# Kernel tuning notes

Measured on AMD Instinct MI355X. Metric: run time of the kernel, lower is better.

The kernel has to match this reference:

```python
import jax, jax.numpy as jnp
import numpy as np

T, H, B = 1024, 512, 64

def setup_inputs() -> dict:
    key = jax.random.key(0)
    ks = jax.random.split(key, 9)
    s = 1.0 / np.sqrt(H)
    inp = {"in_seq": jax.random.normal(ks[0], (T, H, B), dtype=jnp.float32)}
    for i, name in enumerate(["Wxi", "Wxf", "Wxo", "Wxg", "Whi", "Whf", "Who", "Whg"]):
        inp[name] = jax.random.normal(ks[i + 1], (H, H), dtype=jnp.float32) * s
    return inp


def reference(in_seq, Wxi, Wxf, Wxo, Wxg, Whi, Whf, Who, Whg):
    # in_seq: [T, H, B]; x_t, h_t, c_t: [H, B]
    h0 = jnp.zeros_like(in_seq[0])
    c0 = jnp.zeros_like(in_seq[0])

    def step(carry, x):
        h, c = carry
        i = jax.nn.sigmoid(Wxi @ x + Whi @ h)
        f = jax.nn.sigmoid(Wxf @ x + Whf @ h)
        g = jnp.tanh(Wxg @ x + Whg @ h)
        o = jax.nn.sigmoid(Wxo @ x + Who @ h)
        c = f * c + i * g
        h = o * jnp.tanh(c)
        return (h, c), h

    (h, c), outputs = jax.lax.scan(step, (h0, c0), in_seq)
    return outputs, h, c  # outputs: [T, H, B]
```

## Files before the change

kernel.cpp:

```cpp
#include <hip/hip_runtime.h>
#include <hip/hip_bf16.h>

typedef unsigned short u16;
typedef unsigned int   u32;
typedef unsigned long long u64;

typedef __attribute__((ext_vector_type(8))) short short8;
typedef __attribute__((ext_vector_type(4))) float f32x4;
typedef __attribute__((ext_vector_type(4))) u32   u32x4;

#define TT 1024
#define HH 512
#define BB 64
#define GCOLS 8
#define LDSK 528

#define HTB_PAR 16384
#define HTB_GRP 2048

__device__ __forceinline__ u16 f2bf(float f) {
    union { float f; u32 u; } v; v.f = f;
    u32 u = v.u;
    return (u16)((u + 0x7FFFu + ((u >> 16) & 1u)) >> 16);
}

__device__ __forceinline__ short8 cvt8(const float4 &a, const float4 &b) {
    short8 r;
    r[0] = (short)f2bf(a.x); r[1] = (short)f2bf(a.y);
    r[2] = (short)f2bf(a.z); r[3] = (short)f2bf(a.w);
    r[4] = (short)f2bf(b.x); r[5] = (short)f2bf(b.y);
    r[6] = (short)f2bf(b.z); r[7] = (short)f2bf(b.w);
    return r;
}

__device__ __forceinline__ float fast_rcp(float x) {
    float r; asm("v_rcp_f32 %0, %1" : "=v"(r) : "v"(x)); return r;
}
__device__ __forceinline__ float fast_sigmoid(float x) {
    return fast_rcp(1.f + __expf(-x));
}
__device__ __forceinline__ float fast_tanh(float x) {
    float e = __expf(2.f * x);
    return 1.f - 2.f * fast_rcp(e + 1.f);
}

__device__ __forceinline__ void barrier_lgkm() {
    asm volatile("s_waitcnt lgkmcnt(0)" ::: "memory");
    __builtin_amdgcn_s_barrier();
}

__device__ __forceinline__ void load4_llc(const u64* p, u32x4 &A, u32x4 &B, u32x4 &C, u32x4 &D) {
    asm volatile(
        "global_load_dwordx4 %0, %4, off sc0 sc1\n\t"
        "global_load_dwordx4 %1, %4, off offset:16 sc0 sc1\n\t"
        "global_load_dwordx4 %2, %4, off offset:32 sc0 sc1\n\t"
        "global_load_dwordx4 %3, %4, off offset:48 sc0 sc1\n\t"
        "s_waitcnt vmcnt(0)"
        : "=&v"(A), "=&v"(B), "=&v"(C), "=&v"(D) : "v"(p) : "memory");
}
__device__ __forceinline__ void store_llc(u64* p, u64 v) {
    asm volatile("global_store_dwordx2 %0, %1, off sc0 sc1" :: "v"(p), "v"(v) : "memory");
}

__global__ void lstm_prep(u64* htb) {
    int i = blockIdx.x * 256 + threadIdx.x;
    __hip_atomic_store(&htb[i], 0ull, __ATOMIC_RELAXED, __HIP_MEMORY_SCOPE_AGENT);
}

__global__ __launch_bounds__(256, 1)
void lstm_persist(const float* __restrict__ in_seq,
                  const float* __restrict__ Wxi, const float* __restrict__ Wxf,
                  const float* __restrict__ Wxo, const float* __restrict__ Wxg,
                  const float* __restrict__ Whi, const float* __restrict__ Whf,
                  const float* __restrict__ Who, const float* __restrict__ Whg,
                  float* __restrict__ out, u64* htb)
{
    __shared__ u16 xt[2][16][LDSK];
    __shared__ u16 htl[16][LDSK];

    const int tid  = threadIdx.x;
    const int bid  = blockIdx.x;
    const int g    = bid & 7;
    const int rblk = bid >> 3;
    const int wave = tid >> 6;
    const int lane = tid & 63;
    const int lrow = lane & 15;
    const int lk8  = (lane >> 4) * 8;

    {
        u16* p0 = &xt[0][0][0]; u16* p1 = &htl[0][0];
        for (int i = tid; i < 2 * 16 * LDSK; i += 256) p0[i] = 0;
        for (int i = tid; i < 16 * LDSK; i += 256) p1[i] = 0;
    }

    const int gt   = lrow & 3;
    const int grow = rblk * 16 + wave * 4 + (lrow >> 2);
    const float* WxS = (gt == 0) ? Wxi : (gt == 1) ? Wxf : (gt == 2) ? Wxo : Wxg;
    const float* WhS = (gt == 0) ? Whi : (gt == 1) ? Whf : (gt == 2) ? Who : Whg;

    short8 afrag[32];
    #pragma unroll
    for (int kk = 0; kk < 16; ++kk) {
        const float* s = WxS + grow * HH + kk * 32 + lk8;
        afrag[kk] = cvt8(*(const float4*)s, *(const float4*)(s + 4));
    }
    #pragma unroll
    for (int kk = 0; kk < 16; ++kk) {
        const float* s = WhS + grow * HH + kk * 32 + lk8;
        afrag[16 + kk] = cvt8(*(const float4*)s, *(const float4*)(s + 4));
    }

    const int q    = lane >> 4;
    const int colv = lrow;
    const int hid  = rblk * 16 + wave * 4 + q;
    float cst = 0.f;
    float hv_prev = 0.f;

    const int sc   = tid >> 5;
    const int sk0  = (tid & 31) * 16;
    const int soff = g * HTB_GRP + sc * 256 + (tid & 31) * 8;
    const int doff = g * HTB_GRP + colv * 256 + (hid >> 1);

    float4 a0, a1, b0, b1;
    {
        const float* xb = in_seq + (size_t)(tid * 2) * BB + g * GCOLS;
        a0 = *(const float4*)(xb);      a1 = *(const float4*)(xb + 4);
        b0 = *(const float4*)(xb + BB); b1 = *(const float4*)(xb + BB + 4);
        int k = tid * 2;
        const float *ra = (const float*)&a0, *rb = (const float*)&b0;
        #pragma unroll
        for (int j = 0; j < 4; ++j)
            *(u32*)&xt[0][j][k] = (u32)f2bf(ra[j]) | ((u32)f2bf(rb[j]) << 16);
        const float *ra1 = (const float*)&a1, *rb1 = (const float*)&b1;
        #pragma unroll
        for (int j = 0; j < 4; ++j)
            *(u32*)&xt[0][4 + j][k] = (u32)f2bf(ra1[j]) | ((u32)f2bf(rb1[j]) << 16);
    }
    __syncthreads();

    for (int t = 0; t < TT; ++t) {
        f32x4 aA = {0.f, 0.f, 0.f, 0.f}, aB = {0.f, 0.f, 0.f, 0.f};
        {
            const u16 (*xc)[LDSK] = xt[t & 1];
            #pragma unroll
            for (int kk = 0; kk < 8; ++kk) {
                short8 bfr = *(const short8*)&xc[lrow][kk * 32 + lk8];
                aA = __builtin_amdgcn_mfma_f32_16x16x32_bf16(afrag[kk], bfr, aA, 0, 0, 0);
            }
            #pragma unroll
            for (int kk = 8; kk < 16; ++kk) {
                short8 bfr = *(const short8*)&xc[lrow][kk * 32 + lk8];
                aB = __builtin_amdgcn_mfma_f32_16x16x32_bf16(afrag[kk], bfr, aB, 0, 0, 0);
            }
        }

        if (t > 0) {
            const u64* pC = htb + (t & 1) * HTB_PAR + soff;
            const u32 want = (u32)t;
            u32x4 A, B, C, D;
            bool got = false;
            do {
                load4_llc(pC, A, B, C, D);
                got = (A[1] == want) & (A[3] == want) & (B[1] == want) & (B[3] == want) &
                      (C[1] == want) & (C[3] == want) & (D[1] == want) & (D[3] == want);
            } while (!got);

            if (colv < 8)
                out[(size_t)(t - 1) * (HH * BB) + hid * BB + g * GCOLS + colv] = hv_prev;

            u32x4 lo, hi;
            lo[0] = A[0]; lo[1] = A[2]; lo[2] = B[0]; lo[3] = B[2];
            hi[0] = C[0]; hi[1] = C[2]; hi[2] = D[0]; hi[3] = D[2];
            *(u32x4*)&htl[sc][sk0]     = lo;
            *(u32x4*)&htl[sc][sk0 + 8] = hi;
        }

        if (t + 1 < TT) {
            const float* xb = in_seq + (size_t)(t + 1) * (HH * BB)
                            + (size_t)(tid * 2) * BB + g * GCOLS;
            a0 = *(const float4*)(xb);      a1 = *(const float4*)(xb + 4);
            b0 = *(const float4*)(xb + BB); b1 = *(const float4*)(xb + BB + 4);
        }
        barrier_lgkm();

        f32x4 aC = {0.f, 0.f, 0.f, 0.f}, aD = {0.f, 0.f, 0.f, 0.f};
        #pragma unroll
        for (int kk = 0; kk < 8; ++kk) {
            short8 bfr = *(const short8*)&htl[lrow][kk * 32 + lk8];
            aC = __builtin_amdgcn_mfma_f32_16x16x32_bf16(afrag[16 + kk], bfr, aC, 0, 0, 0);
        }
        #pragma unroll
        for (int kk = 8; kk < 16; ++kk) {
            short8 bfr = *(const short8*)&htl[lrow][kk * 32 + lk8];
            aD = __builtin_amdgcn_mfma_f32_16x16x32_bf16(afrag[16 + kk], bfr, aD, 0, 0, 0);
        }
        f32x4 acc = (aA + aB) + (aC + aD);

        if (colv < 8) {
            float iv = fast_sigmoid(acc[0]);
            float fv = fast_sigmoid(acc[1]);
            float ov = fast_sigmoid(acc[2]);
            float gv = fast_tanh(acc[3]);
            cst = fv * cst + iv * gv;
            float hv = ov * fast_tanh(cst);

            u16 hb = f2bf(hv);
            u32 up = (u32)__shfl_down((int)(u32)hb, 16);
            if ((q & 1) == 0) {
                u64 pack = ((u64)(u32)(t + 1) << 32) | ((u64)(up & 0xffffu) << 16) | (u64)hb;
                store_llc(htb + ((t + 1) & 1) * HTB_PAR + doff, pack);
            }
            hv_prev = hv;
            if (t == TT - 1) {
                size_t base = (size_t)TT * HH * BB;
                out[base + hid * BB + g * GCOLS + colv] = hv;
                out[base + HH * BB + hid * BB + g * GCOLS + colv] = cst;
            }
        }

        if (t + 1 < TT) {
            int k = tid * 2;
            u16 (*xn)[LDSK] = xt[(t + 1) & 1];
            const float *ra = (const float*)&a0, *rb = (const float*)&b0;
            #pragma unroll
            for (int j = 0; j < 4; ++j)
                *(u32*)&xn[j][k] = (u32)f2bf(ra[j]) | ((u32)f2bf(rb[j]) << 16);
            const float *ra1 = (const float*)&a1, *rb1 = (const float*)&b1;
            #pragma unroll
            for (int j = 0; j < 4; ++j)
                *(u32*)&xn[4 + j][k] = (u32)f2bf(ra1[j]) | ((u32)f2bf(rb1[j]) << 16);
        }
        barrier_lgkm();
    }

    if (colv < 8)
        out[(size_t)(TT - 1) * (HH * BB) + hid * BB + g * GCOLS + colv] = hv_prev;
}

extern "C" void kernel_launch(void* const* d_in, const int* in_sizes, int n_in,
                              void* d_out, int out_size, void* d_ws, size_t ws_size,
                              hipStream_t stream)
{
    const float* in_seq = (const float*)d_in[0];
    const float* Wxi = (const float*)d_in[1];
    const float* Wxf = (const float*)d_in[2];
    const float* Wxo = (const float*)d_in[3];
    const float* Wxg = (const float*)d_in[4];
    const float* Whi = (const float*)d_in[5];
    const float* Whf = (const float*)d_in[6];
    const float* Who = (const float*)d_in[7];
    const float* Whg = (const float*)d_in[8];

    u64* htb = (u64*)d_ws;

    lstm_prep<<<128, 256, 0, stream>>>(htb);
    lstm_persist<<<256, 256, 0, stream>>>(in_seq, Wxi, Wxf, Wxo, Wxg,
                                          Whi, Whf, Who, Whg,
                                          (float*)d_out, htb);
}
```

Before: 2.599 ms.

## Replace mid-step barrier with per-chunk LDS flags for fine-grained h consumption

```diff
diff --git a/kernel.cpp b/kernel.cpp
--- a/kernel.cpp
+++ b/kernel.cpp
@@ -13,7 +13,7 @@
 #define HH 512
 #define BB 64
 #define GCOLS 8
-#define LDSK 528
+#define LDSK 520
 
 #define HTB_PAR 16384
 #define HTB_GRP 2048
@@ -44,27 +44,22 @@
     return 1.f - 2.f * fast_rcp(e + 1.f);
 }
 
-__device__ __forceinline__ void barrier_lgkm() {
-    asm volatile("s_waitcnt lgkmcnt(0)" ::: "memory");
-    __builtin_amdgcn_s_barrier();
-}
-
-__device__ __forceinline__ void load4_llc(const u64* p, u32x4 &A, u32x4 &B, u32x4 &C, u32x4 &D) {
+__device__ __forceinline__ void poll_issue(const u64* p, u32x4 &A, u32x4 &B, u32x4 &C, u32x4 &D) {
     asm volatile(
         "global_load_dwordx4 %0, %4, off sc0 sc1\n\t"
-        "global_load_dwordx4 %1, %4, off offset:16 sc0 sc1\n\t"
-        "global_load_dwordx4 %2, %4, off offset:32 sc0 sc1\n\t"
-        "global_load_dwordx4 %3, %4, off offset:48 sc0 sc1\n\t"
-        "s_waitcnt vmcnt(0)"
-        : "=&v"(A), "=&v"(B), "=&v"(C), "=&v"(D) : "v"(p) : "memory");
+        "global_load_dwordx4 %1, %4, off offset:128 sc0 sc1\n\t"
+        "global_load_dwordx4 %2, %4, off offset:256 sc0 sc1\n\t"
+        "global_load_dwordx4 %3, %4, off offset:384 sc0 sc1"
+        : "=&v"(A), "=&v"(B), "=&v"(C), "=&v"(D)
+        : "v"(p)
+        : "memory");
+}
+__device__ __forceinline__ void poll_wait(u32x4 &A, u32x4 &B, u32x4 &C, u32x4 &D) {
+    asm volatile("s_waitcnt vmcnt(0)"
+        : "+v"(A), "+v"(B), "+v"(C), "+v"(D) :: "memory");
 }
 __device__ __forceinline__ void store_llc(u64* p, u64 v) {
     asm volatile("global_store_dwordx2 %0, %1, off sc0 sc1" :: "v"(p), "v"(v) : "memory");
-}
-
-__global__ void lstm_prep(u64* htb) {
-    int i = blockIdx.x * 256 + threadIdx.x;
-    __hip_atomic_store(&htb[i], 0ull, __ATOMIC_RELAXED, __HIP_MEMORY_SCOPE_AGENT);
 }
 
 __global__ __launch_bounds__(256, 1)
@@ -76,25 +71,26 @@
                   float* __restrict__ out, u64* htb)
 {
     __shared__ u16 xt[2][16][LDSK];
-    __shared__ u16 htl[16][LDSK];
+    __shared__ u16 htl[2][16][LDSK];
+    __shared__ u32 hflag[16];
 
     const int tid  = threadIdx.x;
     const int bid  = blockIdx.x;
     const int g    = bid & 7;
     const int rblk = bid >> 3;
-    const int wave = tid >> 6;
+    const int wv   = tid >> 6;
     const int lane = tid & 63;
     const int lrow = lane & 15;
     const int lk8  = (lane >> 4) * 8;
 
     {
-        u16* p0 = &xt[0][0][0]; u16* p1 = &htl[0][0];
-        for (int i = tid; i < 2 * 16 * LDSK; i += 256) p0[i] = 0;
-        for (int i = tid; i < 16 * LDSK; i += 256) p1[i] = 0;
+        u16* p0 = &xt[0][0][0]; u16* p1 = &htl[0][0][0];
+        for (int i = tid; i < 2 * 16 * LDSK; i += 256) { p0[i] = 0; p1[i] = 0; }
+        if (tid < 16) hflag[tid] = 0;
     }
 
     const int gt   = lrow & 3;
-    const int grow = rblk * 16 + wave * 4 + (lrow >> 2);
+    const int grow = rblk * 16 + wv * 4 + (lrow >> 2);
     const float* WxS = (gt == 0) ? Wxi : (gt == 1) ? Wxf : (gt == 2) ? Wxo : Wxg;
     const float* WhS = (gt == 0) ? Whi : (gt == 1) ? Whf : (gt == 2) ? Who : Whg;
 
@@ -105,21 +101,21 @@
         afrag[kk] = cvt8(*(const float4*)s, *(const float4*)(s + 4));
     }
     #pragma unroll
-    for (int kk = 0; kk < 16; ++kk) {
+    for (int i = 0; i < 16; ++i) {
+        int kk = (4 * wv + i) & 15;
         const float* s = WhS + grow * HH + kk * 32 + lk8;
-        afrag[16 + kk] = cvt8(*(const float4*)s, *(const float4*)(s + 4));
+        afrag[16 + i] = cvt8(*(const float4*)s, *(const float4*)(s + 4));
     }
 
     const int q    = lane >> 4;
     const int colv = lrow;
-    const int hid  = rblk * 16 + wave * 4 + q;
+    const int hid  = rblk * 16 + wv * 4 + q;
     float cst = 0.f;
-    float hv_prev = 0.f;
-
-    const int sc   = tid >> 5;
-    const int sk0  = (tid & 31) * 16;
-    const int soff = g * HTB_GRP + sc * 256 + (tid & 31) * 8;
-    const int doff = g * HTB_GRP + colv * 256 + (hid >> 1);
+
+    const int pc    = lane >> 3;
+    const int pm    = lane & 7;
+    const int poffb = g * HTB_GRP + pc * 256 + 64 * wv + 2 * pm;
+    const int doff  = g * HTB_GRP + colv * 256 + (hid >> 1);
 
     float4 a0, a1, b0, b1;
     {
@@ -139,9 +135,11 @@
     __syncthreads();
 
     for (int t = 0; t < TT; ++t) {
+        const int par = t & 1;
+
         f32x4 aA = {0.f, 0.f, 0.f, 0.f}, aB = {0.f, 0.f, 0.f, 0.f};
         {
-            const u16 (*xc)[LDSK] = xt[t & 1];
+            const u16 (*xc)[LDSK] = xt[par];
             #pragma unroll
             for (int kk = 0; kk < 8; ++kk) {
                 short8 bfr = *(const short8*)&xc[lrow][kk * 32 + lk8];
@@ -155,24 +153,41 @@
         }
 
         if (t > 0) {
-            const u64* pC = htb + (t & 1) * HTB_PAR + soff;
             const u32 want = (u32)t;
-            u32x4 A, B, C, D;
-            bool got = false;
+            const u64* p = htb + par * HTB_PAR + poffb;
+            int pend = 0xF;
             do {
-                load4_llc(pC, A, B, C, D);
-                got = (A[1] == want) & (A[3] == want) & (B[1] == want) & (B[3] == want) &
-                      (C[1] == want) & (C[3] == want) & (D[1] == want) & (D[3] == want);
-            } while (!got);
-
-            if (colv < 8)
-                out[(size_t)(t - 1) * (HH * BB) + hid * BB + g * GCOLS + colv] = hv_prev;
-
-            u32x4 lo, hi;
-            lo[0] = A[0]; lo[1] = A[2]; lo[2] = B[0]; lo[3] = B[2];
-            hi[0] = C[0]; hi[1] = C[2]; hi[2] = D[0]; hi[3] = D[2];
-            *(u32x4*)&htl[sc][sk0]     = lo;
-            *(u32x4*)&htl[sc][sk0 + 8] = hi;
+                u32x4 v0, v1, v2, v3;
+                poll_issue(p, v0, v1, v2, v3);
+                poll_wait(v0, v1, v2, v3);
+                int newly = 0;
+                if (pend & 1) if (__all((v0[1] == want) & (v0[3] == want))) {
+                    *(u64*)&htl[par][pc][32 * (4 * wv + 0) + 4 * pm] = (u64)v0[0] | ((u64)v0[2] << 32);
+                    newly |= 1;
+                }
+                if (pend & 2) if (__all((v1[1] == want) & (v1[3] == want))) {
+                    *(u64*)&htl[par][pc][32 * (4 * wv + 1) + 4 * pm] = (u64)v1[0] | ((u64)v1[2] << 32);
+                    newly |= 2;
+                }
+                if (pend & 4) if (__all((v2[1] == want) & (v2[3] == want))) {
+                    *(u64*)&htl[par][pc][32 * (4 * wv + 2) + 4 * pm] = (u64)v2[0] | ((u64)v2[2] << 32);
+                    newly |= 4;
+                }
+                if (pend & 8) if (__all((v3[1] == want) & (v3[3] == want))) {
+                    *(u64*)&htl[par][pc][32 * (4 * wv + 3) + 4 * pm] = (u64)v3[0] | ((u64)v3[2] << 32);
+                    newly |= 8;
+                }
+                if (newly) {
+                    asm volatile("s_waitcnt lgkmcnt(0)" ::: "memory");
+                    if (lane == 0) {
+                        if (newly & 1) __hip_atomic_store(&hflag[4 * wv + 0], want, __ATOMIC_RELAXED, __HIP_MEMORY_SCOPE_WORKGROUP);
+                        if (newly & 2) __hip_atomic_store(&hflag[4 * wv + 1], want, __ATOMIC_RELAXED, __HIP_MEMORY_SCOPE_WORKGROUP);
+                        if (newly & 4) __hip_atomic_store(&hflag[4 * wv + 2], want, __ATOMIC_RELAXED, __HIP_MEMORY_SCOPE_WORKGROUP);
+                        if (newly & 8) __hip_atomic_store(&hflag[4 * wv + 3], want, __ATOMIC_RELAXED, __HIP_MEMORY_SCOPE_WORKGROUP);
+                    }
+                    pend &= ~newly;
+                }
+            } while (pend);
         }
 
         if (t + 1 < TT) {
@@ -181,18 +196,28 @@
             a0 = *(const float4*)(xb);      a1 = *(const float4*)(xb + 4);
             b0 = *(const float4*)(xb + BB); b1 = *(const float4*)(xb + BB + 4);
         }
-        barrier_lgkm();
 
         f32x4 aC = {0.f, 0.f, 0.f, 0.f}, aD = {0.f, 0.f, 0.f, 0.f};
-        #pragma unroll
-        for (int kk = 0; kk < 8; ++kk) {
-            short8 bfr = *(const short8*)&htl[lrow][kk * 32 + lk8];
-            aC = __builtin_amdgcn_mfma_f32_16x16x32_bf16(afrag[16 + kk], bfr, aC, 0, 0, 0);
-        }
-        #pragma unroll
-        for (int kk = 8; kk < 16; ++kk) {
-            short8 bfr = *(const short8*)&htl[lrow][kk * 32 + lk8];
-            aD = __builtin_amdgcn_mfma_f32_16x16x32_bf16(afrag[16 + kk], bfr, aD, 0, 0, 0);
+        if (t > 0) {
+            const u32 want = (u32)t;
+            const u16 (*hc)[LDSK] = htl[par];
+#define HCHUNK(I)                                                                          \
+            {                                                                              \
+                int kk = (4 * wv + (I)) & 15;                                              \
+                if ((I) >= 4) {                                                            \
+                    while (__hip_atomic_load(&hflag[kk], __ATOMIC_RELAXED,                 \
+                                             __HIP_MEMORY_SCOPE_WORKGROUP) != want) {}     \
+                    asm volatile("" ::: "memory");                                         \
+                }                                                                          \
+                short8 bfr = *(const short8*)&hc[lrow][kk * 32 + lk8];                     \
+                if ((I) & 1) aD = __builtin_amdgcn_mfma_f32_16x16x32_bf16(afrag[16 + (I)], bfr, aD, 0, 0, 0); \
+                else         aC = __builtin_amdgcn_mfma_f32_16x16x32_bf16(afrag[16 + (I)], bfr, aC, 0, 0, 0); \
+            }
+            HCHUNK(0)  HCHUNK(1)  HCHUNK(2)  HCHUNK(3)
+            HCHUNK(4)  HCHUNK(5)  HCHUNK(6)  HCHUNK(7)
+            HCHUNK(8)  HCHUNK(9)  HCHUNK(10) HCHUNK(11)
+            HCHUNK(12) HCHUNK(13) HCHUNK(14) HCHUNK(15)
+#undef HCHUNK
         }
         f32x4 acc = (aA + aB) + (aC + aD);
 
@@ -210,7 +235,7 @@
                 u64 pack = ((u64)(u32)(t + 1) << 32) | ((u64)(up & 0xffffu) << 16) | (u64)hb;
                 store_llc(htb + ((t + 1) & 1) * HTB_PAR + doff, pack);
             }
-            hv_prev = hv;
+            out[(size_t)t * (HH * BB) + hid * BB + g * GCOLS + colv] = hv;
             if (t == TT - 1) {
                 size_t base = (size_t)TT * HH * BB;
                 out[base + hid * BB + g * GCOLS + colv] = hv;
@@ -230,11 +255,9 @@
             for (int j = 0; j < 4; ++j)
                 *(u32*)&xn[4 + j][k] = (u32)f2bf(ra1[j]) | ((u32)f2bf(rb1[j]) << 16);
         }
-        barrier_lgkm();
-    }
-
-    if (colv < 8)
-        out[(size_t)(TT - 1) * (HH * BB) + hid * BB + g * GCOLS + colv] = hv_prev;
+
+        __syncthreads();
+    }
 }
 
 extern "C" void kernel_launch(void* const* d_in, const int* in_sizes, int n_in,
@@ -253,7 +276,6 @@
 
     u64* htb = (u64*)d_ws;
 
-    lstm_prep<<<128, 256, 0, stream>>>(htb);
     lstm_persist<<<256, 256, 0, stream>>>(in_seq, Wxi, Wxf, Wxo, Wxg,
                                           Whi, Whf, Who, Whg,
                                           (float*)d_out, htb);
```

Result: faster. 2.461 ms (-5.3%).

## Replace block barriers with per-quarter LDS flags and double-buffer hidden state

Applied to the files above, without the earlier changes.

```diff
diff --git a/kernel.cpp b/kernel.cpp
--- a/kernel.cpp
+++ b/kernel.cpp
@@ -36,27 +36,33 @@
 __device__ __forceinline__ float fast_rcp(float x) {
     float r; asm("v_rcp_f32 %0, %1" : "=v"(r) : "v"(x)); return r;
 }
-__device__ __forceinline__ float fast_sigmoid(float x) {
-    return fast_rcp(1.f + __expf(-x));
-}
+__device__ __forceinline__ float fast_sigmoid(float x) { return fast_rcp(1.f + __expf(-x)); }
 __device__ __forceinline__ float fast_tanh(float x) {
     float e = __expf(2.f * x);
     return 1.f - 2.f * fast_rcp(e + 1.f);
 }
 
-__device__ __forceinline__ void barrier_lgkm() {
-    asm volatile("s_waitcnt lgkmcnt(0)" ::: "memory");
-    __builtin_amdgcn_s_barrier();
-}
-
-__device__ __forceinline__ void load4_llc(const u64* p, u32x4 &A, u32x4 &B, u32x4 &C, u32x4 &D) {
+__device__ __forceinline__ void quad_spin(const u32* fl, int qb, u32 want) {
+    u32 f0, f1, f2, f3;
+    do {
+        f0 = __hip_atomic_load(&fl[qb + 0], __ATOMIC_RELAXED, __HIP_MEMORY_SCOPE_WORKGROUP);
+        f1 = __hip_atomic_load(&fl[qb + 1], __ATOMIC_RELAXED, __HIP_MEMORY_SCOPE_WORKGROUP);
+        f2 = __hip_atomic_load(&fl[qb + 2], __ATOMIC_RELAXED, __HIP_MEMORY_SCOPE_WORKGROUP);
+        f3 = __hip_atomic_load(&fl[qb + 3], __ATOMIC_RELAXED, __HIP_MEMORY_SCOPE_WORKGROUP);
+    } while (((int)(f0 - want) | (int)(f1 - want) | (int)(f2 - want) | (int)(f3 - want)) < 0);
+    asm volatile("" ::: "memory");
+}
+
+__device__ __forceinline__ void poll_issue(const u64* p, u32x4 &A, u32x4 &B, u32x4 &C, u32x4 &D) {
     asm volatile(
         "global_load_dwordx4 %0, %4, off sc0 sc1\n\t"
-        "global_load_dwordx4 %1, %4, off offset:16 sc0 sc1\n\t"
-        "global_load_dwordx4 %2, %4, off offset:32 sc0 sc1\n\t"
-        "global_load_dwordx4 %3, %4, off offset:48 sc0 sc1\n\t"
-        "s_waitcnt vmcnt(0)"
+        "global_load_dwordx4 %1, %4, off offset:128 sc0 sc1\n\t"
+        "global_load_dwordx4 %2, %4, off offset:256 sc0 sc1\n\t"
+        "global_load_dwordx4 %3, %4, off offset:384 sc0 sc1"
         : "=&v"(A), "=&v"(B), "=&v"(C), "=&v"(D) : "v"(p) : "memory");
+}
+__device__ __forceinline__ void poll_wait(u32x4 &A, u32x4 &B, u32x4 &C, u32x4 &D) {
+    asm volatile("s_waitcnt vmcnt(0)" : "+v"(A), "+v"(B), "+v"(C), "+v"(D) :: "memory");
 }
 __device__ __forceinline__ void store_llc(u64* p, u64 v) {
     asm volatile("global_store_dwordx2 %0, %1, off sc0 sc1" :: "v"(p), "v"(v) : "memory");
@@ -76,162 +82,206 @@
                   float* __restrict__ out, u64* htb)
 {
     __shared__ u16 xt[2][16][LDSK];
-    __shared__ u16 htl[16][LDSK];
+    __shared__ u16 htl[2][16][LDSK];
+    __shared__ u32 xflag[16];
+    __shared__ u32 hflag[16];
 
     const int tid  = threadIdx.x;
     const int bid  = blockIdx.x;
     const int g    = bid & 7;
     const int rblk = bid >> 3;
-    const int wave = tid >> 6;
+    const int wv   = tid >> 6;
     const int lane = tid & 63;
     const int lrow = lane & 15;
     const int lk8  = (lane >> 4) * 8;
 
     {
-        u16* p0 = &xt[0][0][0]; u16* p1 = &htl[0][0];
-        for (int i = tid; i < 2 * 16 * LDSK; i += 256) p0[i] = 0;
-        for (int i = tid; i < 16 * LDSK; i += 256) p1[i] = 0;
+        u16* p0 = &xt[0][0][0]; u16* p1 = &htl[0][0][0];
+        for (int i = tid; i < 2 * 16 * LDSK; i += 256) { p0[i] = 0; p1[i] = 0; }
+        if (tid < 16) { xflag[tid] = 1; hflag[tid] = 0; }
     }
 
     const int gt   = lrow & 3;
-    const int grow = rblk * 16 + wave * 4 + (lrow >> 2);
+    const int grow = rblk * 16 + wv * 4 + (lrow >> 2);
     const float* WxS = (gt == 0) ? Wxi : (gt == 1) ? Wxf : (gt == 2) ? Wxo : Wxg;
     const float* WhS = (gt == 0) ? Whi : (gt == 1) ? Whf : (gt == 2) ? Who : Whg;
 
     short8 afrag[32];
     #pragma unroll
-    for (int kk = 0; kk < 16; ++kk) {
-        const float* s = WxS + grow * HH + kk * 32 + lk8;
-        afrag[kk] = cvt8(*(const float4*)s, *(const float4*)(s + 4));
-    }
-    #pragma unroll
-    for (int kk = 0; kk < 16; ++kk) {
-        const float* s = WhS + grow * HH + kk * 32 + lk8;
-        afrag[16 + kk] = cvt8(*(const float4*)s, *(const float4*)(s + 4));
-    }
+    for (int J = 0; J < 4; ++J)
+        #pragma unroll
+        for (int i = 0; i < 4; ++i) {
+            int kk = 4 * ((wv + J) & 3) + i;
+            const float* sx = WxS + grow * HH + kk * 32 + lk8;
+            const float* sh = WhS + grow * HH + kk * 32 + lk8;
+            afrag[4 * J + i]      = cvt8(*(const float4*)sx, *(const float4*)(sx + 4));
+            afrag[16 + 4 * J + i] = cvt8(*(const float4*)sh, *(const float4*)(sh + 4));
+        }
 
     const int q    = lane >> 4;
     const int colv = lrow;
-    const int hid  = rblk * 16 + wave * 4 + q;
+    const int hid  = rblk * 16 + wv * 4 + q;
     float cst = 0.f;
     float hv_prev = 0.f;
 
-    const int sc   = tid >> 5;
-    const int sk0  = (tid & 31) * 16;
-    const int soff = g * HTB_GRP + sc * 256 + (tid & 31) * 8;
-    const int doff = g * HTB_GRP + colv * 256 + (hid >> 1);
-
-    float4 a0, a1, b0, b1;
+    const int pc    = lane >> 3;
+    const int pm    = lane & 7;
+    const int poffb = g * HTB_GRP + pc * 256 + 64 * wv + 2 * pm;
+    const int doff  = g * HTB_GRP + colv * 256 + (hid >> 1);
+
+    float4 xA0, xA1, xA2, xA3, xB0, xB1, xB2, xB3;
     {
         const float* xb = in_seq + (size_t)(tid * 2) * BB + g * GCOLS;
-        a0 = *(const float4*)(xb);      a1 = *(const float4*)(xb + 4);
-        b0 = *(const float4*)(xb + BB); b1 = *(const float4*)(xb + BB + 4);
+        float4 c0 = *(const float4*)(xb);      float4 c1 = *(const float4*)(xb + 4);
+        float4 c2 = *(const float4*)(xb + BB); float4 c3 = *(const float4*)(xb + BB + 4);
         int k = tid * 2;
-        const float *ra = (const float*)&a0, *rb = (const float*)&b0;
+        const float *ra = (const float*)&c0, *rb = (const float*)&c2;
         #pragma unroll
         for (int j = 0; j < 4; ++j)
             *(u32*)&xt[0][j][k] = (u32)f2bf(ra[j]) | ((u32)f2bf(rb[j]) << 16);
-        const float *ra1 = (const float*)&a1, *rb1 = (const float*)&b1;
+        const float *ra1 = (const float*)&c1, *rb1 = (const float*)&c3;
         #pragma unroll
         for (int j = 0; j < 4; ++j)
             *(u32*)&xt[0][4 + j][k] = (u32)f2bf(ra1[j]) | ((u32)f2bf(rb1[j]) << 16);
     }
     __syncthreads();
-
-    for (int t = 0; t < TT; ++t) {
-        f32x4 aA = {0.f, 0.f, 0.f, 0.f}, aB = {0.f, 0.f, 0.f, 0.f};
-        {
-            const u16 (*xc)[LDSK] = xt[t & 1];
-            #pragma unroll
-            for (int kk = 0; kk < 8; ++kk) {
-                short8 bfr = *(const short8*)&xc[lrow][kk * 32 + lk8];
-                aA = __builtin_amdgcn_mfma_f32_16x16x32_bf16(afrag[kk], bfr, aA, 0, 0, 0);
-            }
-            #pragma unroll
-            for (int kk = 8; kk < 16; ++kk) {
-                short8 bfr = *(const short8*)&xc[lrow][kk * 32 + lk8];
-                aB = __builtin_amdgcn_mfma_f32_16x16x32_bf16(afrag[kk], bfr, aB, 0, 0, 0);
-            }
-        }
-
-        if (t > 0) {
-            const u64* pC = htb + (t & 1) * HTB_PAR + soff;
-            const u32 want = (u32)t;
-            u32x4 A, B, C, D;
-            bool got = false;
-            do {
-                load4_llc(pC, A, B, C, D);
-                got = (A[1] == want) & (A[3] == want) & (B[1] == want) & (B[3] == want) &
-                      (C[1] == want) & (C[3] == want) & (D[1] == want) & (D[3] == want);
-            } while (!got);
-
-            if (colv < 8)
-                out[(size_t)(t - 1) * (HH * BB) + hid * BB + g * GCOLS + colv] = hv_prev;
-
-            u32x4 lo, hi;
-            lo[0] = A[0]; lo[1] = A[2]; lo[2] = B[0]; lo[3] = B[2];
-            hi[0] = C[0]; hi[1] = C[2]; hi[2] = D[0]; hi[3] = D[2];
-            *(u32x4*)&htl[sc][sk0]     = lo;
-            *(u32x4*)&htl[sc][sk0 + 8] = hi;
-        }
-
-        if (t + 1 < TT) {
-            const float* xb = in_seq + (size_t)(t + 1) * (HH * BB)
-                            + (size_t)(tid * 2) * BB + g * GCOLS;
-            a0 = *(const float4*)(xb);      a1 = *(const float4*)(xb + 4);
-            b0 = *(const float4*)(xb + BB); b1 = *(const float4*)(xb + BB + 4);
-        }
-        barrier_lgkm();
-
-        f32x4 aC = {0.f, 0.f, 0.f, 0.f}, aD = {0.f, 0.f, 0.f, 0.f};
-        #pragma unroll
-        for (int kk = 0; kk < 8; ++kk) {
-            short8 bfr = *(const short8*)&htl[lrow][kk * 32 + lk8];
-            aC = __builtin_amdgcn_mfma_f32_16x16x32_bf16(afrag[16 + kk], bfr, aC, 0, 0, 0);
-        }
-        #pragma unroll
-        for (int kk = 8; kk < 16; ++kk) {
-            short8 bfr = *(const short8*)&htl[lrow][kk * 32 + lk8];
-            aD = __builtin_amdgcn_mfma_f32_16x16x32_bf16(afrag[16 + kk], bfr, aD, 0, 0, 0);
-        }
-        f32x4 acc = (aA + aB) + (aC + aD);
-
-        if (colv < 8) {
-            float iv = fast_sigmoid(acc[0]);
-            float fv = fast_sigmoid(acc[1]);
-            float ov = fast_sigmoid(acc[2]);
-            float gv = fast_tanh(acc[3]);
-            cst = fv * cst + iv * gv;
-            float hv = ov * fast_tanh(cst);
-
-            u16 hb = f2bf(hv);
-            u32 up = (u32)__shfl_down((int)(u32)hb, 16);
-            if ((q & 1) == 0) {
-                u64 pack = ((u64)(u32)(t + 1) << 32) | ((u64)(up & 0xffffu) << 16) | (u64)hb;
-                store_llc(htb + ((t + 1) & 1) * HTB_PAR + doff, pack);
-            }
-            hv_prev = hv;
-            if (t == TT - 1) {
-                size_t base = (size_t)TT * HH * BB;
-                out[base + hid * BB + g * GCOLS + colv] = hv;
-                out[base + HH * BB + hid * BB + g * GCOLS + colv] = cst;
-            }
-        }
-
-        if (t + 1 < TT) {
-            int k = tid * 2;
-            u16 (*xn)[LDSK] = xt[(t + 1) & 1];
-            const float *ra = (const float*)&a0, *rb = (const float*)&b0;
-            #pragma unroll
-            for (int j = 0; j < 4; ++j)
-                *(u32*)&xn[j][k] = (u32)f2bf(ra[j]) | ((u32)f2bf(rb[j]) << 16);
-            const float *ra1 = (const float*)&a1, *rb1 = (const float*)&b1;
-            #pragma unroll
-            for (int j = 0; j < 4; ++j)
-                *(u32*)&xn[4 + j][k] = (u32)f2bf(ra1[j]) | ((u32)f2bf(rb1[j]) << 16);
-        }
-        barrier_lgkm();
-    }
+    {
+        const float* xb = in_seq + (size_t)(HH * BB) + (size_t)(tid * 2) * BB + g * GCOLS;
+        xA0 = *(const float4*)(xb);      xA1 = *(const float4*)(xb + 4);
+        xA2 = *(const float4*)(xb + BB); xA3 = *(const float4*)(xb + BB + 4);
+    }
+
+#define LSTM_STEP(T, RIN0, RIN1, RIN2, RIN3, ROUT0, ROUT1, ROUT2, ROUT3)                      \
+    {                                                                                         \
+        const int t_ = (T);                                                                   \
+        const int par_ = t_ & 1;                                                              \
+                             \
+        f32x4 aA = {0.f,0.f,0.f,0.f}, aB = {0.f,0.f,0.f,0.f};                                 \
+        {                                                                                     \
+            const u32 wantx = (u32)(t_ + 1);                                                  \
+            const u16 (*xc)[LDSK] = xt[par_];                                                 \
+            _Pragma("unroll")                                                                 \
+            for (int J = 0; J < 4; ++J) {                                                     \
+                const int qb = 4 * ((wv + J) & 3);                                            \
+                if (J > 0) quad_spin(xflag, qb, wantx);                                       \
+                short8 b0 = *(const short8*)&xc[lrow][(qb + 0) * 32 + lk8];                   \
+                short8 b1 = *(const short8*)&xc[lrow][(qb + 1) * 32 + lk8];                   \
+                short8 b2 = *(const short8*)&xc[lrow][(qb + 2) * 32 + lk8];                   \
+                short8 b3 = *(const short8*)&xc[lrow][(qb + 3) * 32 + lk8];                   \
+                aA = __builtin_amdgcn_mfma_f32_16x16x32_bf16(afrag[4*J+0], b0, aA, 0, 0, 0);  \
+                aB = __builtin_amdgcn_mfma_f32_16x16x32_bf16(afrag[4*J+1], b1, aB, 0, 0, 0);  \
+                aA = __builtin_amdgcn_mfma_f32_16x16x32_bf16(afrag[4*J+2], b2, aA, 0, 0, 0);  \
+                aB = __builtin_amdgcn_mfma_f32_16x16x32_bf16(afrag[4*J+3], b3, aB, 0, 0, 0);  \
+            }                                                                                 \
+        }                                                                                     \
+                 \
+        if (t_ > 0) {                                                                         \
+            const u32 want = (u32)t_;                                                         \
+            const u64* p_ = htb + par_ * HTB_PAR + poffb;                                     \
+            int pend = 0xF;                                                                   \
+            do {                                                                              \
+                u32x4 v0, v1, v2, v3;                                                         \
+                poll_issue(p_, v0, v1, v2, v3);                                               \
+                poll_wait(v0, v1, v2, v3);                                                    \
+                int newly = 0;                                                                \
+                if ((pend & 1) && __all((v0[1] == want) & (v0[3] == want))) {                 \
+                    *(u64*)&htl[par_][pc][32*(4*wv+0) + 4*pm] = (u64)v0[0] | ((u64)v0[2] << 32); newly |= 1; } \
+                if ((pend & 2) && __all((v1[1] == want) & (v1[3] == want))) {                 \
+                    *(u64*)&htl[par_][pc][32*(4*wv+1) + 4*pm] = (u64)v1[0] | ((u64)v1[2] << 32); newly |= 2; } \
+                if ((pend & 4) && __all((v2[1] == want) & (v2[3] == want))) {                 \
+                    *(u64*)&htl[par_][pc][32*(4*wv+2) + 4*pm] = (u64)v2[0] | ((u64)v2[2] << 32); newly |= 4; } \
+                if ((pend & 8) && __all((v3[1] == want) & (v3[3] == want))) {                 \
+                    *(u64*)&htl[par_][pc][32*(4*wv+3) + 4*pm] = (u64)v3[0] | ((u64)v3[2] << 32); newly |= 8; } \
+                if (newly) {                                                                  \
+                    asm volatile("s_waitcnt lgkmcnt(0)" ::: "memory");                        \
+                    if (lane == 0) {                                                          \
+                        if (newly & 1) __hip_atomic_store(&hflag[4*wv+0], want, __ATOMIC_RELAXED, __HIP_MEMORY_SCOPE_WORKGROUP); \
+                        if (newly & 2) __hip_atomic_store(&hflag[4*wv+1], want, __ATOMIC_RELAXED, __HIP_MEMORY_SCOPE_WORKGROUP); \
+                        if (newly & 4) __hip_atomic_store(&hflag[4*wv+2], want, __ATOMIC_RELAXED, __HIP_MEMORY_SCOPE_WORKGROUP); \
+                        if (newly & 8) __hip_atomic_store(&hflag[4*wv+3], want, __ATOMIC_RELAXED, __HIP_MEMORY_SCOPE_WORKGROUP); \
+                    }                                                                         \
+                    pend &= ~newly;                                                           \
+                }                                                                             \
+            } while (pend);                                                                   \
+            if (colv < 8)                                                                     \
+                out[(size_t)(t_ - 1) * (HH * BB) + hid * BB + g * GCOLS + colv] = hv_prev;    \
+        }                                                                                     \
+                                          \
+        if (t_ + 2 < TT) {                                                                    \
+            const float* xb_ = in_seq + (size_t)(t_ + 2) * (HH * BB)                          \
+                             + (size_t)(tid * 2) * BB + g * GCOLS;                            \
+            ROUT0 = *(const float4*)(xb_);      ROUT1 = *(const float4*)(xb_ + 4);            \
+            ROUT2 = *(const float4*)(xb_ + BB); ROUT3 = *(const float4*)(xb_ + BB + 4);       \
+        }                                                                                     \
+                                                       \
+        f32x4 aC = {0.f,0.f,0.f,0.f}, aD = {0.f,0.f,0.f,0.f};                                 \
+        if (t_ > 0) {                                                                         \
+            const u32 want = (u32)t_;                                                         \
+            const u16 (*hc)[LDSK] = htl[par_];                                                \
+            _Pragma("unroll")                                                                 \
+            for (int J = 0; J < 4; ++J) {                                                     \
+                const int qb = 4 * ((wv + J) & 3);                                            \
+                if (J > 0) quad_spin(hflag, qb, want);                                        \
+                short8 b0 = *(const short8*)&hc[lrow][(qb + 0) * 32 + lk8];                   \
+                short8 b1 = *(const short8*)&hc[lrow][(qb + 1) * 32 + lk8];                   \
+                short8 b2 = *(const short8*)&hc[lrow][(qb + 2) * 32 + lk8];                   \
+                short8 b3 = *(const short8*)&hc[lrow][(qb + 3) * 32 + lk8];                   \
+                aC = __builtin_amdgcn_mfma_f32_16x16x32_bf16(afrag[16+4*J+0], b0, aC, 0, 0, 0); \
+                aD = __builtin_amdgcn_mfma_f32_16x16x32_bf16(afrag[16+4*J+1], b1, aD, 0, 0, 0); \
+                aC = __builtin_amdgcn_mfma_f32_16x16x32_bf16(afrag[16+4*J+2], b2, aC, 0, 0, 0); \
+                aD = __builtin_amdgcn_mfma_f32_16x16x32_bf16(afrag[16+4*J+3], b3, aD, 0, 0, 0); \
+            }                                                                                 \
+        }                                                                                     \
+        f32x4 acc = (aA + aB) + (aC + aD);                                                    \
+                                             \
+        if (colv < 8) {                                                                       \
+            float iv = fast_sigmoid(acc[0]);                                                  \
+            float fv = fast_sigmoid(acc[1]);                                                  \
+            float ov = fast_sigmoid(acc[2]);                                                  \
+            float gv = fast_tanh(acc[3]);                                                     \
+            cst = fv * cst + iv * gv;                                                         \
+            float hv = ov * fast_tanh(cst);                                                   \
+            u16 hb = f2bf(hv);                                                                \
+            u32 up = (u32)__shfl_down((int)(u32)hb, 16);                                      \
+            if ((q & 1) == 0) {                                                               \
+                u64 pack = ((u64)(u32)(t_ + 1) << 32) | ((u64)(up & 0xffffu) << 16) | (u64)hb;\
+                store_llc(htb + ((t_ + 1) & 1) * HTB_PAR + doff, pack);                       \
+            }                                                                                 \
+            hv_prev = hv;                                                                     \
+            if (t_ == TT - 1) {                                                               \
+                size_t base_ = (size_t)TT * HH * BB;                                          \
+                out[base_ + hid * BB + g * GCOLS + colv] = hv;                                \
+                out[base_ + HH * BB + hid * BB + g * GCOLS + colv] = cst;                     \
+            }                                                                                 \
+        }                                                                                     \
+                        \
+        if (t_ + 1 < TT) {                                                                    \
+            int k = tid * 2;                                                                  \
+            u16 (*xn)[LDSK] = xt[(t_ + 1) & 1];                                               \
+            const float *ra = (const float*)&RIN0, *rb = (const float*)&RIN2;                 \
+            _Pragma("unroll")                                                                 \
+            for (int j = 0; j < 4; ++j)                                                       \
+                *(u32*)&xn[j][k] = (u32)f2bf(ra[j]) | ((u32)f2bf(rb[j]) << 16);               \
+            const float *ra1 = (const float*)&RIN1, *rb1 = (const float*)&RIN3;               \
+            _Pragma("unroll")                                                                 \
+            for (int j = 0; j < 4; ++j)                                                       \
+                *(u32*)&xn[4 + j][k] = (u32)f2bf(ra1[j]) | ((u32)f2bf(rb1[j]) << 16);         \
+            asm volatile("s_waitcnt lgkmcnt(0)" ::: "memory");                                \
+            if (lane == 0) {                                                                  \
+                u32 nf = (u32)(t_ + 2);                                                       \
+                __hip_atomic_store(&xflag[4*wv+0], nf, __ATOMIC_RELAXED, __HIP_MEMORY_SCOPE_WORKGROUP); \
+                __hip_atomic_store(&xflag[4*wv+1], nf, __ATOMIC_RELAXED, __HIP_MEMORY_SCOPE_WORKGROUP); \
+                __hip_atomic_store(&xflag[4*wv+2], nf, __ATOMIC_RELAXED, __HIP_MEMORY_SCOPE_WORKGROUP); \
+                __hip_atomic_store(&xflag[4*wv+3], nf, __ATOMIC_RELAXED, __HIP_MEMORY_SCOPE_WORKGROUP); \
+            }                                                                                 \
+        }                                                                                     \
+    }
+
+    for (int t = 0; t < TT; t += 2) {
+        LSTM_STEP(t,     xA0, xA1, xA2, xA3, xB0, xB1, xB2, xB3)
+        LSTM_STEP(t + 1, xB0, xB1, xB2, xB3, xA0, xA1, xA2, xA3)
+    }
+#undef LSTM_STEP
 
     if (colv < 8)
         out[(size_t)(TT - 1) * (HH * BB) + hid * BB + g * GCOLS + colv] = hv_prev;
```

After: 2.183 ms. -16.0%, faster.
